# Kernel optimization log

Hardware: AMD Instinct MI355X
Metric: run time of the kernel (lower is better)

The kernel has to match this reference:

```python
import jax, jax.numpy as jnp
import numpy as np

HID = 2560
NH, P, N, G, K = 80, 64, 128, 1, 4
INTER = NH * P            # 5120
CONV_DIM = INTER + 2 * G * N  # 5376
PROJ = INTER + CONV_DIM + NH  # 10576
EPS = 1e-5
DT_MIN, DT_MAX = 0.0, 100.0
BATCH = 64


def setup_inputs() -> dict:
    key = jax.random.key(0)
    ks = jax.random.split(key, 11)
    return {
        "input_states": jax.random.normal(ks[0], (BATCH, 1, HID), jnp.float32),
        "conv_state": 0.1 * jax.random.normal(ks[1], (BATCH, CONV_DIM, K), jnp.float32),
        "ssm_state": 0.1 * jax.random.normal(ks[2], (BATCH, NH, P, N), jnp.float32),
        "in_proj_w": jax.random.normal(ks[3], (PROJ, HID), jnp.float32) * (HID ** -0.5),
        "conv_w": jax.random.normal(ks[4], (CONV_DIM, K), jnp.float32) * 0.2,
        "conv_b": jax.random.normal(ks[5], (CONV_DIM,), jnp.float32) * 0.02,
        "dt_bias": jax.random.normal(ks[6], (NH,), jnp.float32) * 0.1,
        "A_log": jnp.log(jnp.arange(1, NH + 1, dtype=jnp.float32)),
        "D": jnp.ones((NH,), jnp.float32),
        "norm_w": jnp.ones((INTER,), jnp.float32),
        "out_proj_w": jax.random.normal(ks[7], (HID, INTER), jnp.float32) * (INTER ** -0.5),
    }


def reference(input_states, conv_state, ssm_state, in_proj_w, conv_w, conv_b,
              dt_bias, A_log, D, norm_w, out_proj_w):
    B = input_states.shape[0]
    # in_proj: (B,1,HID) @ (HID,PROJ) -> (B,1,PROJ); d_mlp == 0 with these dims
    proj = jnp.einsum("bsh,ph->bsp", input_states, in_proj_w)
    gate = proj[..., :INTER]                       # (B,1,INTER)
    hBC = proj[..., INTER:INTER + CONV_DIM]        # (B,1,CONV_DIM)
    dt = proj[..., INTER + CONV_DIM:]              # (B,1,NH)

    # conv cache update: roll left, append current token
    new_conv_state = jnp.concatenate(
        [conv_state[:, :, 1:], hBC[:, 0, :, None]], axis=-1)  # (B,CONV_DIM,K)
    x = jnp.sum(new_conv_state * conv_w[None], axis=-1) + conv_b  # (B,CONV_DIM)
    x = jax.nn.silu(x)

    hs = x[:, :INTER].reshape(B, NH, P)            # (B,NH,P)
    Bm = x[:, INTER:INTER + G * N].reshape(B, G, N)
    Cm = x[:, INTER + G * N:].reshape(B, G, N)
    Bm = jnp.repeat(Bm, NH // G, axis=1)           # (B,NH,N)
    Cm = jnp.repeat(Cm, NH // G, axis=1)           # (B,NH,N)

    # discretization (dt is per-head, broadcast over head_dim as in source)
    dt_sp = jnp.clip(jax.nn.softplus(dt[:, 0, :] + dt_bias), DT_MIN, DT_MAX)  # (B,NH)
    A = -jnp.exp(A_log)                            # (NH,)
    dA = jnp.exp(dt_sp * A)                        # (B,NH)

    dBx = dt_sp[:, :, None, None] * Bm[:, :, None, :] * hs[..., None]  # (B,NH,P,N)
    new_ssm = ssm_state * dA[:, :, None, None] + dBx                   # (B,NH,P,N)

    y = jnp.einsum("bhpn,bhn->bhp", new_ssm, Cm)   # (B,NH,P)
    y = y + hs * D[None, :, None]
    y = y.reshape(B, 1, INTER)

    # gated RMSNorm (fp32 internals)
    yf = y.astype(jnp.float32) * jax.nn.silu(gate.astype(jnp.float32))
    var = jnp.mean(yf * yf, axis=-1, keepdims=True)
    yn = norm_w * (yf * jax.lax.rsqrt(var + EPS)).astype(y.dtype)

    out = jnp.einsum("bsi,hi->bsh", yn, out_proj_w)  # (B,1,HID)
    return out
```

## Files before the change

### kernel.cpp

```cpp
#include <hip/hip_runtime.h>
#include <stdint.h>

#define HID 2560
#define NH 80
#define PDIM 64
#define NDIM 128
#define INTER 5120
#define CONV_DIM 5376
#define PROJ_DIM 10576
#define NBATCH 64
#define EPS_ 1e-5f

typedef short short8 __attribute__((ext_vector_type(8)));
typedef float f32x4 __attribute__((ext_vector_type(4)));

__device__ __forceinline__ unsigned short f2bf(float f){
  unsigned u = __builtin_bit_cast(unsigned, f);
  u += 0x7FFFu + ((u >> 16) & 1u);
  return (unsigned short)(u >> 16);
}
__device__ __forceinline__ float silu_(float x){ return x / (1.f + __expf(-x)); }

__global__ __launch_bounds__(256) void k_dt(const float* __restrict__ X,
                                            const float* __restrict__ W,
                                            float* __restrict__ dt_part,
                                            unsigned short* __restrict__ Xb){
  const int h = blockIdx.x, ks = blockIdx.y;
  const int tid = threadIdx.x, wid = tid >> 6, lane = tid & 63;
  const float* wr = W + (size_t)(INTER + CONV_DIM + h) * HID + ks * 320;
  float w[5];
  #pragma unroll
  for (int i = 0; i < 5; ++i) w[i] = wr[lane + i * 64];
  #pragma unroll
  for (int bi = 0; bi < 16; ++bi){
    const int b = wid * 16 + bi;
    const float* xr = X + (size_t)b * HID + ks * 320;
    float x[5];
    float acc = 0.f;
    #pragma unroll
    for (int i = 0; i < 5; ++i){ x[i] = xr[lane + i * 64]; acc += x[i] * w[i]; }
    if (h == 0){
      #pragma unroll
      for (int i = 0; i < 5; ++i)
        Xb[(size_t)b * HID + ks * 320 + lane + i * 64] = f2bf(x[i]);
    }
    #pragma unroll
    for (int m = 32; m; m >>= 1) acc += __shfl_xor(acc, m);
    if (lane == 0) dt_part[(ks * NBATCH + b) * NH + h] = acc;
  }
}

__global__ __launch_bounds__(64, 1) void k1_proj(const unsigned short* __restrict__ Xb,
                                                 const float* __restrict__ W,
                                                 float* __restrict__ pp){
  const int lane = threadIdx.x;
  const int lr = lane & 15, lg = lane >> 4;
  const int n0 = blockIdx.x * 64;
  const int ks = blockIdx.y;
  const int kb = ks * 320;
  const short* ap = (const short*)Xb + (size_t)lr * HID + kb + lg * 8;
  const float* bp0; const float* bp1; const float* bp2; const float* bp3;
  {
    int r0 = n0;          if (r0 > PROJ_DIM - 16) r0 = PROJ_DIM - 16;
    int r1 = n0 + 16;     if (r1 > PROJ_DIM - 16) r1 = PROJ_DIM - 16;
    int r2 = n0 + 32;     if (r2 > PROJ_DIM - 16) r2 = PROJ_DIM - 16;
    int r3 = n0 + 48;     if (r3 > PROJ_DIM - 16) r3 = PROJ_DIM - 16;
    bp0 = W + (size_t)(r0 + lr) * HID + kb + lg * 8;
    bp1 = W + (size_t)(r1 + lr) * HID + kb + lg * 8;
    bp2 = W + (size_t)(r2 + lr) * HID + kb + lg * 8;
    bp3 = W + (size_t)(r3 + lr) * HID + kb + lg * 8;
  }
  f32x4 acc0[4], acc1[4], acc2[4], acc3[4];
  #pragma unroll
  for (int mt = 0; mt < 4; ++mt){
    acc0[mt] = (f32x4){0,0,0,0}; acc1[mt] = (f32x4){0,0,0,0};
    acc2[mt] = (f32x4){0,0,0,0}; acc3[mt] = (f32x4){0,0,0,0};
  }
  short8 A0[2], A1[2], A2[2], A3[2];
  float4 Bv0[2][2], Bv1[2][2], Bv2[2][2], Bv3[2][2];
  A0[0] = *(const short8*)(ap);
  A1[0] = *(const short8*)(ap + 16 * HID);
  A2[0] = *(const short8*)(ap + 32 * HID);
  A3[0] = *(const short8*)(ap + 48 * HID);
  Bv0[0][0] = *(const float4*)(bp0); Bv0[0][1] = *(const float4*)(bp0 + 4);
  Bv1[0][0] = *(const float4*)(bp1); Bv1[0][1] = *(const float4*)(bp1 + 4);
  Bv2[0][0] = *(const float4*)(bp2); Bv2[0][1] = *(const float4*)(bp2 + 4);
  Bv3[0][0] = *(const float4*)(bp3); Bv3[0][1] = *(const float4*)(bp3 + 4);
  #pragma unroll
  for (int s = 0; s < 10; ++s){
    const int p = s & 1;
    if (s + 1 < 10){
      const int k = (s + 1) * 32, q = p ^ 1;
      A0[q] = *(const short8*)(ap + k);
      A1[q] = *(const short8*)(ap + 16 * HID + k);
      A2[q] = *(const short8*)(ap + 32 * HID + k);
      A3[q] = *(const short8*)(ap + 48 * HID + k);
      Bv0[q][0] = *(const float4*)(bp0 + k); Bv0[q][1] = *(const float4*)(bp0 + k + 4);
      Bv1[q][0] = *(const float4*)(bp1 + k); Bv1[q][1] = *(const float4*)(bp1 + k + 4);
      Bv2[q][0] = *(const float4*)(bp2 + k); Bv2[q][1] = *(const float4*)(bp2 + k + 4);
      Bv3[q][0] = *(const float4*)(bp3 + k); Bv3[q][1] = *(const float4*)(bp3 + k + 4);
    }
    short8 bb0, bb1, bb2, bb3;
    bb0[0]=(short)f2bf(Bv0[p][0].x); bb0[1]=(short)f2bf(Bv0[p][0].y);
    bb0[2]=(short)f2bf(Bv0[p][0].z); bb0[3]=(short)f2bf(Bv0[p][0].w);
    bb0[4]=(short)f2bf(Bv0[p][1].x); bb0[5]=(short)f2bf(Bv0[p][1].y);
    bb0[6]=(short)f2bf(Bv0[p][1].z); bb0[7]=(short)f2bf(Bv0[p][1].w);
    bb1[0]=(short)f2bf(Bv1[p][0].x); bb1[1]=(short)f2bf(Bv1[p][0].y);
    bb1[2]=(short)f2bf(Bv1[p][0].z); bb1[3]=(short)f2bf(Bv1[p][0].w);
    bb1[4]=(short)f2bf(Bv1[p][1].x); bb1[5]=(short)f2bf(Bv1[p][1].y);
    bb1[6]=(short)f2bf(Bv1[p][1].z); bb1[7]=(short)f2bf(Bv1[p][1].w);
    bb2[0]=(short)f2bf(Bv2[p][0].x); bb2[1]=(short)f2bf(Bv2[p][0].y);
    bb2[2]=(short)f2bf(Bv2[p][0].z); bb2[3]=(short)f2bf(Bv2[p][0].w);
    bb2[4]=(short)f2bf(Bv2[p][1].x); bb2[5]=(short)f2bf(Bv2[p][1].y);
    bb2[6]=(short)f2bf(Bv2[p][1].z); bb2[7]=(short)f2bf(Bv2[p][1].w);
    bb3[0]=(short)f2bf(Bv3[p][0].x); bb3[1]=(short)f2bf(Bv3[p][0].y);
    bb3[2]=(short)f2bf(Bv3[p][0].z); bb3[3]=(short)f2bf(Bv3[p][0].w);
    bb3[4]=(short)f2bf(Bv3[p][1].x); bb3[5]=(short)f2bf(Bv3[p][1].y);
    bb3[6]=(short)f2bf(Bv3[p][1].z); bb3[7]=(short)f2bf(Bv3[p][1].w);
    acc0[0] = __builtin_amdgcn_mfma_f32_16x16x32_bf16(A0[p], bb0, acc0[0], 0, 0, 0);
    acc0[1] = __builtin_amdgcn_mfma_f32_16x16x32_bf16(A1[p], bb0, acc0[1], 0, 0, 0);
    acc0[2] = __builtin_amdgcn_mfma_f32_16x16x32_bf16(A2[p], bb0, acc0[2], 0, 0, 0);
    acc0[3] = __builtin_amdgcn_mfma_f32_16x16x32_bf16(A3[p], bb0, acc0[3], 0, 0, 0);
    acc1[0] = __builtin_amdgcn_mfma_f32_16x16x32_bf16(A0[p], bb1, acc1[0], 0, 0, 0);
    acc1[1] = __builtin_amdgcn_mfma_f32_16x16x32_bf16(A1[p], bb1, acc1[1], 0, 0, 0);
    acc1[2] = __builtin_amdgcn_mfma_f32_16x16x32_bf16(A2[p], bb1, acc1[2], 0, 0, 0);
    acc1[3] = __builtin_amdgcn_mfma_f32_16x16x32_bf16(A3[p], bb1, acc1[3], 0, 0, 0);
    acc2[0] = __builtin_amdgcn_mfma_f32_16x16x32_bf16(A0[p], bb2, acc2[0], 0, 0, 0);
    acc2[1] = __builtin_amdgcn_mfma_f32_16x16x32_bf16(A1[p], bb2, acc2[1], 0, 0, 0);
    acc2[2] = __builtin_amdgcn_mfma_f32_16x16x32_bf16(A2[p], bb2, acc2[2], 0, 0, 0);
    acc2[3] = __builtin_amdgcn_mfma_f32_16x16x32_bf16(A3[p], bb2, acc2[3], 0, 0, 0);
    acc3[0] = __builtin_amdgcn_mfma_f32_16x16x32_bf16(A0[p], bb3, acc3[0], 0, 0, 0);
    acc3[1] = __builtin_amdgcn_mfma_f32_16x16x32_bf16(A1[p], bb3, acc3[1], 0, 0, 0);
    acc3[2] = __builtin_amdgcn_mfma_f32_16x16x32_bf16(A2[p], bb3, acc3[2], 0, 0, 0);
    acc3[3] = __builtin_amdgcn_mfma_f32_16x16x32_bf16(A3[p], bb3, acc3[3], 0, 0, 0);
  }
  float* plane = pp + (size_t)ks * NBATCH * PROJ_DIM;
  #pragma unroll
  for (int mt = 0; mt < 4; ++mt){
    #pragma unroll
    for (int r = 0; r < 4; ++r){
      const int m = mt * 16 + lg * 4 + r;
      float* pm = plane + (size_t)m * PROJ_DIM;
      if (n0      < PROJ_DIM) pm[n0      + lr] = acc0[mt][r];
      if (n0 + 16 < PROJ_DIM) pm[n0 + 16 + lr] = acc1[mt][r];
      if (n0 + 32 < PROJ_DIM) pm[n0 + 32 + lr] = acc2[mt][r];
      if (n0 + 48 < PROJ_DIM) pm[n0 + 48 + lr] = acc3[mt][r];
    }
  }
}

__global__ __launch_bounds__(256) void k2a(const float* __restrict__ cs,
                                           const float* __restrict__ cw,
                                           const float* __restrict__ cb,
                                           const float* __restrict__ pp,
                                           const float* __restrict__ dt_part,
                                           const float* __restrict__ dt_bias,
                                           const float* __restrict__ A_log,
                                           float* __restrict__ hs_bc,
                                           float* __restrict__ dt_sp,
                                           float* __restrict__ dAv,
                                           float* __restrict__ s_bc){
  const int b = blockIdx.y;
  const int c0 = blockIdx.x * 384;
  const int tid = threadIdx.x;
  const size_t plane = (size_t)NBATCH * PROJ_DIM;
  __shared__ float bc[384];
  for (int i = tid; i < 384; i += 256){
    const int c = c0 + i;
    float4 s4 = *(const float4*)(cs + ((size_t)b * CONV_DIM + c) * 4);
    float4 w4 = *(const float4*)(cw + (size_t)c * 4);
    const size_t pidx = (size_t)b * PROJ_DIM + INTER + c;
    float hbc = 0.f;
    #pragma unroll
    for (int ks = 0; ks < 8; ++ks) hbc += pp[(size_t)ks * plane + pidx];
    float x = s4.y * w4.x + s4.z * w4.y + s4.w * w4.z + hbc * w4.w + cb[c];
    float v = silu_(x);
    hs_bc[(size_t)b * CONV_DIM + c] = v;
    if (blockIdx.x == 13) bc[i] = v;
  }
  if (blockIdx.x == 0 && tid < NH){
    float acc = dt_bias[tid];
    #pragma unroll
    for (int ks = 0; ks < 8; ++ks) acc += dt_part[(ks * NBATCH + b) * NH + tid];
    float sp = acc > 15.f ? acc : log1pf(__expf(acc));
    sp = fminf(fmaxf(sp, 0.f), 100.f);
    dt_sp[b * NH + tid] = sp;
    dAv[b * NH + tid] = __expf(-sp * __expf(A_log[tid]));
  }
  if (blockIdx.x == 13){
    __syncthreads();
    if (tid < 64){
      float p = bc[128 + tid] * bc[256 + tid] + bc[192 + tid] * bc[320 + tid];
      #pragma unroll
      for (int m = 32; m; m >>= 1) p += __shfl_xor(p, m);
      if (tid == 0) s_bc[b] = p;
    }
  }
}

__global__ __launch_bounds__(256) void k2b(const float* __restrict__ ssm,
                                           const float* __restrict__ hs_bc,
                                           const float* __restrict__ pp,
                                           const float* __restrict__ dt_sp,
                                           const float* __restrict__ dAv,
                                           const float* __restrict__ s_bc,
                                           const float* __restrict__ Dp,
                                           const float* __restrict__ norm_w,
                                           unsigned short* __restrict__ yfb,
                                           float* __restrict__ ssq_part){
  const int h = blockIdx.x, b = blockIdx.y;
  const int tid = threadIdx.x;
  const int wid = tid >> 6, lane = tid & 63;
  const int lr = lane & 15, lg = lane >> 4;
  const float dA_s = dAv[b * NH + h];
  const float coef = dt_sp[b * NH + h] * s_bc[b] + Dp[h];
  const size_t plane = (size_t)NBATCH * PROJ_DIM;
  const float* Cb = hs_bc + (size_t)b * CONV_DIM + INTER + NDIM;
  float4 c0 = *(const float4*)(Cb + lr * 8);
  float4 c1 = *(const float4*)(Cb + lr * 8 + 4);
  const float* srow = ssm + ((size_t)b * NH + h) * PDIM * NDIM;
  float ssq = 0.f;
  __shared__ float ssql[4];
  #pragma unroll
  for (int r = 0; r < 4; ++r){
    const int p = wid * 16 + r * 4 + lg;
    const float* sp_ = srow + (size_t)p * NDIM + lr * 8;
    float4 v0 = *(const float4*)(sp_);
    float4 v1 = *(const float4*)(sp_ + 4);
    float dot = v0.x*c0.x + v0.y*c0.y + v0.z*c0.z + v0.w*c0.w
              + v1.x*c1.x + v1.y*c1.y + v1.z*c1.z + v1.w*c1.w;
    dot += __shfl_xor(dot, 1); dot += __shfl_xor(dot, 2);
    dot += __shfl_xor(dot, 4); dot += __shfl_xor(dot, 8);
    if (lr == 0){
      const int hp = h * PDIM + p;
      float hs = hs_bc[(size_t)b * CONV_DIM + hp];
      float y = dA_s * dot + hs * coef;
      const size_t gi = (size_t)b * PROJ_DIM + hp;
      float g = 0.f;
      #pragma unroll
      for (int ks = 0; ks < 8; ++ks) g += pp[(size_t)ks * plane + gi];
      float yf = y * silu_(g) * norm_w[hp];
      yfb[(size_t)b * INTER + hp] = f2bf(yf);
      ssq += yf * yf;
    }
  }
  #pragma unroll
  for (int m = 32; m; m >>= 1) ssq += __shfl_xor(ssq, m);
  if (lane == 0) ssql[wid] = ssq;
  __syncthreads();
  if (tid == 0) ssq_part[b * NH + h] = ssql[0] + ssql[1] + ssql[2] + ssql[3];
}

__global__ __launch_bounds__(64, 1) void k3_out(const unsigned short* __restrict__ Yb,
                                                const float* __restrict__ W,
                                                float* __restrict__ part){
  const int lane = threadIdx.x;
  const int lr = lane & 15, lg = lane >> 4;
  const int n0 = blockIdx.x * 32;
  const int ks = blockIdx.y;
  const int kb = ks * 320;
  const short* ap = (const short*)Yb + (size_t)lr * INTER + kb + lg * 8;
  const float* bp0 = W + (size_t)(n0      + lr) * INTER + kb + lg * 8;
  const float* bp1 = W + (size_t)(n0 + 16 + lr) * INTER + kb + lg * 8;
  f32x4 acc0[4], acc1[4];
  #pragma unroll
  for (int mt = 0; mt < 4; ++mt){
    acc0[mt] = (f32x4){0,0,0,0}; acc1[mt] = (f32x4){0,0,0,0};
  }
  short8 A0[2], A1[2], A2[2], A3[2];
  float4 Bv0[2][2], Bv1[2][2];
  A0[0] = *(const short8*)(ap);
  A1[0] = *(const short8*)(ap + 16 * INTER);
  A2[0] = *(const short8*)(ap + 32 * INTER);
  A3[0] = *(const short8*)(ap + 48 * INTER);
  Bv0[0][0] = *(const float4*)(bp0); Bv0[0][1] = *(const float4*)(bp0 + 4);
  Bv1[0][0] = *(const float4*)(bp1); Bv1[0][1] = *(const float4*)(bp1 + 4);
  #pragma unroll
  for (int s = 0; s < 10; ++s){
    const int p = s & 1;
    if (s + 1 < 10){
      const int k = (s + 1) * 32, q = p ^ 1;
      A0[q] = *(const short8*)(ap + k);
      A1[q] = *(const short8*)(ap + 16 * INTER + k);
      A2[q] = *(const short8*)(ap + 32 * INTER + k);
      A3[q] = *(const short8*)(ap + 48 * INTER + k);
      Bv0[q][0] = *(const float4*)(bp0 + k); Bv0[q][1] = *(const float4*)(bp0 + k + 4);
      Bv1[q][0] = *(const float4*)(bp1 + k); Bv1[q][1] = *(const float4*)(bp1 + k + 4);
    }
    short8 bb0, bb1;
    bb0[0]=(short)f2bf(Bv0[p][0].x); bb0[1]=(short)f2bf(Bv0[p][0].y);
    bb0[2]=(short)f2bf(Bv0[p][0].z); bb0[3]=(short)f2bf(Bv0[p][0].w);
    bb0[4]=(short)f2bf(Bv0[p][1].x); bb0[5]=(short)f2bf(Bv0[p][1].y);
    bb0[6]=(short)f2bf(Bv0[p][1].z); bb0[7]=(short)f2bf(Bv0[p][1].w);
    bb1[0]=(short)f2bf(Bv1[p][0].x); bb1[1]=(short)f2bf(Bv1[p][0].y);
    bb1[2]=(short)f2bf(Bv1[p][0].z); bb1[3]=(short)f2bf(Bv1[p][0].w);
    bb1[4]=(short)f2bf(Bv1[p][1].x); bb1[5]=(short)f2bf(Bv1[p][1].y);
    bb1[6]=(short)f2bf(Bv1[p][1].z); bb1[7]=(short)f2bf(Bv1[p][1].w);
    acc0[0] = __builtin_amdgcn_mfma_f32_16x16x32_bf16(A0[p], bb0, acc0[0], 0, 0, 0);
    acc0[1] = __builtin_amdgcn_mfma_f32_16x16x32_bf16(A1[p], bb0, acc0[1], 0, 0, 0);
    acc0[2] = __builtin_amdgcn_mfma_f32_16x16x32_bf16(A2[p], bb0, acc0[2], 0, 0, 0);
    acc0[3] = __builtin_amdgcn_mfma_f32_16x16x32_bf16(A3[p], bb0, acc0[3], 0, 0, 0);
    acc1[0] = __builtin_amdgcn_mfma_f32_16x16x32_bf16(A0[p], bb1, acc1[0], 0, 0, 0);
    acc1[1] = __builtin_amdgcn_mfma_f32_16x16x32_bf16(A1[p], bb1, acc1[1], 0, 0, 0);
    acc1[2] = __builtin_amdgcn_mfma_f32_16x16x32_bf16(A2[p], bb1, acc1[2], 0, 0, 0);
    acc1[3] = __builtin_amdgcn_mfma_f32_16x16x32_bf16(A3[p], bb1, acc1[3], 0, 0, 0);
  }
  float* pt = part + (size_t)ks * NBATCH * 2560;
  #pragma unroll
  for (int mt = 0; mt < 4; ++mt){
    #pragma unroll
    for (int r = 0; r < 4; ++r){
      const int m = mt * 16 + lg * 4 + r;
      float* pm = pt + (size_t)m * 2560;
      pm[n0      + lr] = acc0[mt][r];
      pm[n0 + 16 + lr] = acc1[mt][r];
    }
  }
}

__global__ __launch_bounds__(256) void k4_norm(const float* __restrict__ part,
                                               const float* __restrict__ ssq_part,
                                               float* __restrict__ out){
  const int b = blockIdx.y;
  const int tid = threadIdx.x;
  __shared__ float w4[4];
  __shared__ float sc;
  float v = (tid < NH) ? ssq_part[b * NH + tid] : 0.f;
  #pragma unroll
  for (int m = 32; m; m >>= 1) v += __shfl_xor(v, m);
  const int wid = tid >> 6, lane = tid & 63;
  if (lane == 0) w4[wid] = v;
  __syncthreads();
  if (tid == 0){
    float total = w4[0] + w4[1] + w4[2] + w4[3];
    sc = rsqrtf(total / (float)INTER + EPS_);
  }
  __syncthreads();
  const int j = blockIdx.x * 256 + tid;
  const size_t idx = (size_t)b * 2560 + j;
  const size_t plane = (size_t)NBATCH * 2560;
  float s = 0.f;
  #pragma unroll
  for (int ks = 0; ks < 16; ++ks) s += part[(size_t)ks * plane + idx];
  out[idx] = sc * s;
}

extern "C" void kernel_launch(void* const* d_in, const int* in_sizes, int n_in,
                              void* d_out, int out_size, void* d_ws, size_t ws_size,
                              hipStream_t stream){
  const float* x_in       = (const float*)d_in[0];
  const float* conv_state = (const float*)d_in[1];
  const float* ssm_state  = (const float*)d_in[2];
  const float* in_proj_w  = (const float*)d_in[3];
  const float* conv_w     = (const float*)d_in[4];
  const float* conv_b     = (const float*)d_in[5];
  const float* dt_bias    = (const float*)d_in[6];
  const float* A_log      = (const float*)d_in[7];
  const float* Dp         = (const float*)d_in[8];
  const float* norm_w     = (const float*)d_in[9];
  const float* out_proj_w = (const float*)d_in[10];
  float* out = (float*)d_out;

  char* ws = (char*)d_ws;
  unsigned short* Xb   = (unsigned short*)(ws);
  float* dt_part       = (float*)(ws + 327680);
  float* pp            = (float*)(ws + 491520);
  float* hs_bc         = (float*)(ws + 22151168);
  float* dt_sp         = (float*)(ws + 23527424);
  float* dAv           = (float*)(ws + 23547904);
  float* s_bc          = (float*)(ws + 23568384);
  float* ssq           = (float*)(ws + 23568640);
  unsigned short* Yb   = (unsigned short*)(ws + 23589120);
  float* part          = (float*)(ws + 24244480);

  k_dt<<<dim3(NH, 8), dim3(256), 0, stream>>>(x_in, in_proj_w, dt_part, Xb);
  k1_proj<<<dim3(166, 8), dim3(64), 0, stream>>>(Xb, in_proj_w, pp);
  k2a<<<dim3(14, NBATCH), dim3(256), 0, stream>>>(conv_state, conv_w, conv_b, pp,
                                                  dt_part, dt_bias, A_log,
                                                  hs_bc, dt_sp, dAv, s_bc);
  k2b<<<dim3(NH, NBATCH), dim3(256), 0, stream>>>(ssm_state, hs_bc, pp, dt_sp, dAv,
                                                  s_bc, Dp, norm_w, Yb, ssq);
  k3_out<<<dim3(80, 16), dim3(64), 0, stream>>>(Yb, out_proj_w, part);
  k4_norm<<<dim3(10, NBATCH), dim3(256), 0, stream>>>(part, ssq, out);
}
```

Before: 123.7 us.

## Double split-K depth and store GEMM partial sums as bf16

Both projection GEMMs now use twice as many K-splits (16 and 32), so each block does half the K work and the grid has twice as many blocks to fill the GPU. The split-K partial planes are written as bf16 instead of fp32, which halves workspace traffic for the extra partials. The consumer kernels sum 16 or 32 bf16 partials. This trades accuracy, since each partial sum is rounded to bf16 before reduction, for more parallelism and less memory traffic.

```diff
diff --git a/kernel.cpp b/kernel.cpp
--- a/kernel.cpp
+++ b/kernel.cpp
@@ -19,6 +19,10 @@
   u += 0x7FFFu + ((u >> 16) & 1u);
   return (unsigned short)(u >> 16);
 }
+__device__ __forceinline__ float bf2f(unsigned short v){
+  unsigned x = (unsigned)v << 16;
+  return __builtin_bit_cast(float, x);
+}
 __device__ __forceinline__ float silu_(float x){ return x / (1.f + __expf(-x)); }
 
 __global__ __launch_bounds__(256) void k_dt(const float* __restrict__ X,
@@ -52,12 +56,12 @@
 
 __global__ __launch_bounds__(64, 1) void k1_proj(const unsigned short* __restrict__ Xb,
                                                  const float* __restrict__ W,
-                                                 float* __restrict__ pp){
+                                                 unsigned short* __restrict__ pp){
   const int lane = threadIdx.x;
   const int lr = lane & 15, lg = lane >> 4;
   const int n0 = blockIdx.x * 64;
   const int ks = blockIdx.y;
-  const int kb = ks * 320;
+  const int kb = ks * 160;
   const short* ap = (const short*)Xb + (size_t)lr * HID + kb + lg * 8;
   const float* bp0; const float* bp1; const float* bp2; const float* bp3;
   {
@@ -87,9 +91,9 @@
   Bv2[0][0] = *(const float4*)(bp2); Bv2[0][1] = *(const float4*)(bp2 + 4);
   Bv3[0][0] = *(const float4*)(bp3); Bv3[0][1] = *(const float4*)(bp3 + 4);
   #pragma unroll
-  for (int s = 0; s < 10; ++s){
+  for (int s = 0; s < 5; ++s){
     const int p = s & 1;
-    if (s + 1 < 10){
+    if (s + 1 < 5){
       const int k = (s + 1) * 32, q = p ^ 1;
       A0[q] = *(const short8*)(ap + k);
       A1[q] = *(const short8*)(ap + 16 * HID + k);
@@ -134,17 +138,17 @@
     acc3[2] = __builtin_amdgcn_mfma_f32_16x16x32_bf16(A2[p], bb3, acc3[2], 0, 0, 0);
     acc3[3] = __builtin_amdgcn_mfma_f32_16x16x32_bf16(A3[p], bb3, acc3[3], 0, 0, 0);
   }
-  float* plane = pp + (size_t)ks * NBATCH * PROJ_DIM;
+  unsigned short* plane = pp + (size_t)ks * NBATCH * PROJ_DIM;
   #pragma unroll
   for (int mt = 0; mt < 4; ++mt){
     #pragma unroll
     for (int r = 0; r < 4; ++r){
       const int m = mt * 16 + lg * 4 + r;
-      float* pm = plane + (size_t)m * PROJ_DIM;
-      if (n0      < PROJ_DIM) pm[n0      + lr] = acc0[mt][r];
-      if (n0 + 16 < PROJ_DIM) pm[n0 + 16 + lr] = acc1[mt][r];
-      if (n0 + 32 < PROJ_DIM) pm[n0 + 32 + lr] = acc2[mt][r];
-      if (n0 + 48 < PROJ_DIM) pm[n0 + 48 + lr] = acc3[mt][r];
+      unsigned short* pm = plane + (size_t)m * PROJ_DIM;
+      if (n0      < PROJ_DIM) pm[n0      + lr] = f2bf(acc0[mt][r]);
+      if (n0 + 16 < PROJ_DIM) pm[n0 + 16 + lr] = f2bf(acc1[mt][r]);
+      if (n0 + 32 < PROJ_DIM) pm[n0 + 32 + lr] = f2bf(acc2[mt][r]);
+      if (n0 + 48 < PROJ_DIM) pm[n0 + 48 + lr] = f2bf(acc3[mt][r]);
     }
   }
 }
@@ -152,7 +156,7 @@
 __global__ __launch_bounds__(256) void k2a(const float* __restrict__ cs,
                                            const float* __restrict__ cw,
                                            const float* __restrict__ cb,
-                                           const float* __restrict__ pp,
+                                           const unsigned short* __restrict__ pp,
                                            const float* __restrict__ dt_part,
                                            const float* __restrict__ dt_bias,
                                            const float* __restrict__ A_log,
@@ -172,7 +176,7 @@
     const size_t pidx = (size_t)b * PROJ_DIM + INTER + c;
     float hbc = 0.f;
     #pragma unroll
-    for (int ks = 0; ks < 8; ++ks) hbc += pp[(size_t)ks * plane + pidx];
+    for (int ks = 0; ks < 16; ++ks) hbc += bf2f(pp[(size_t)ks * plane + pidx]);
     float x = s4.y * w4.x + s4.z * w4.y + s4.w * w4.z + hbc * w4.w + cb[c];
     float v = silu_(x);
     hs_bc[(size_t)b * CONV_DIM + c] = v;
@@ -200,7 +204,7 @@
 
 __global__ __launch_bounds__(256) void k2b(const float* __restrict__ ssm,
                                            const float* __restrict__ hs_bc,
-                                           const float* __restrict__ pp,
+                                           const unsigned short* __restrict__ pp,
                                            const float* __restrict__ dt_sp,
                                            const float* __restrict__ dAv,
                                            const float* __restrict__ s_bc,
@@ -238,7 +242,7 @@
       const size_t gi = (size_t)b * PROJ_DIM + hp;
       float g = 0.f;
       #pragma unroll
-      for (int ks = 0; ks < 8; ++ks) g += pp[(size_t)ks * plane + gi];
+      for (int ks = 0; ks < 16; ++ks) g += bf2f(pp[(size_t)ks * plane + gi]);
       float yf = y * silu_(g) * norm_w[hp];
       yfb[(size_t)b * INTER + hp] = f2bf(yf);
       ssq += yf * yf;
@@ -253,12 +257,12 @@
 
 __global__ __launch_bounds__(64, 1) void k3_out(const unsigned short* __restrict__ Yb,
                                                 const float* __restrict__ W,
-                                                float* __restrict__ part){
+                                                unsigned short* __restrict__ part){
   const int lane = threadIdx.x;
   const int lr = lane & 15, lg = lane >> 4;
   const int n0 = blockIdx.x * 32;
   const int ks = blockIdx.y;
-  const int kb = ks * 320;
+  const int kb = ks * 160;
   const short* ap = (const short*)Yb + (size_t)lr * INTER + kb + lg * 8;
   const float* bp0 = W + (size_t)(n0      + lr) * INTER + kb + lg * 8;
   const float* bp1 = W + (size_t)(n0 + 16 + lr) * INTER + kb + lg * 8;
@@ -276,9 +280,9 @@
   Bv0[0][0] = *(const float4*)(bp0); Bv0[0][1] = *(const float4*)(bp0 + 4);
   Bv1[0][0] = *(const float4*)(bp1); Bv1[0][1] = *(const float4*)(bp1 + 4);
   #pragma unroll
-  for (int s = 0; s < 10; ++s){
+  for (int s = 0; s < 5; ++s){
     const int p = s & 1;
-    if (s + 1 < 10){
+    if (s + 1 < 5){
       const int k = (s + 1) * 32, q = p ^ 1;
       A0[q] = *(const short8*)(ap + k);
       A1[q] = *(const short8*)(ap + 16 * INTER + k);
@@ -305,20 +309,20 @@
     acc1[2] = __builtin_amdgcn_mfma_f32_16x16x32_bf16(A2[p], bb1, acc1[2], 0, 0, 0);
     acc1[3] = __builtin_amdgcn_mfma_f32_16x16x32_bf16(A3[p], bb1, acc1[3], 0, 0, 0);
   }
-  float* pt = part + (size_t)ks * NBATCH * 2560;
+  unsigned short* pt = part + (size_t)ks * NBATCH * 2560;
   #pragma unroll
   for (int mt = 0; mt < 4; ++mt){
     #pragma unroll
     for (int r = 0; r < 4; ++r){
       const int m = mt * 16 + lg * 4 + r;
-      float* pm = pt + (size_t)m * 2560;
-      pm[n0      + lr] = acc0[mt][r];
-      pm[n0 + 16 + lr] = acc1[mt][r];
-    }
-  }
-}
-
-__global__ __launch_bounds__(256) void k4_norm(const float* __restrict__ part,
+      unsigned short* pm = pt + (size_t)m * 2560;
+      pm[n0      + lr] = f2bf(acc0[mt][r]);
+      pm[n0 + 16 + lr] = f2bf(acc1[mt][r]);
+    }
+  }
+}
+
+__global__ __launch_bounds__(256) void k4_norm(const unsigned short* __restrict__ part,
                                                const float* __restrict__ ssq_part,
                                                float* __restrict__ out){
   const int b = blockIdx.y;
@@ -341,7 +345,7 @@
   const size_t plane = (size_t)NBATCH * 2560;
   float s = 0.f;
   #pragma unroll
-  for (int ks = 0; ks < 16; ++ks) s += part[(size_t)ks * plane + idx];
+  for (int ks = 0; ks < 32; ++ks) s += bf2f(part[(size_t)ks * plane + idx]);
   out[idx] = sc * s;
 }
 
@@ -364,22 +368,22 @@
   char* ws = (char*)d_ws;
   unsigned short* Xb   = (unsigned short*)(ws);
   float* dt_part       = (float*)(ws + 327680);
-  float* pp            = (float*)(ws + 491520);
+  unsigned short* pp   = (unsigned short*)(ws + 491520);
   float* hs_bc         = (float*)(ws + 22151168);
   float* dt_sp         = (float*)(ws + 23527424);
   float* dAv           = (float*)(ws + 23547904);
   float* s_bc          = (float*)(ws + 23568384);
   float* ssq           = (float*)(ws + 23568640);
   unsigned short* Yb   = (unsigned short*)(ws + 23589120);
-  float* part          = (float*)(ws + 24244480);
+  unsigned short* part = (unsigned short*)(ws + 24244480);
 
   k_dt<<<dim3(NH, 8), dim3(256), 0, stream>>>(x_in, in_proj_w, dt_part, Xb);
-  k1_proj<<<dim3(166, 8), dim3(64), 0, stream>>>(Xb, in_proj_w, pp);
+  k1_proj<<<dim3(166, 16), dim3(64), 0, stream>>>(Xb, in_proj_w, pp);
   k2a<<<dim3(14, NBATCH), dim3(256), 0, stream>>>(conv_state, conv_w, conv_b, pp,
                                                   dt_part, dt_bias, A_log,
                                                   hs_bc, dt_sp, dAv, s_bc);
   k2b<<<dim3(NH, NBATCH), dim3(256), 0, stream>>>(ssm_state, hs_bc, pp, dt_sp, dAv,
                                                   s_bc, Dp, norm_w, Yb, ssq);
-  k3_out<<<dim3(80, 16), dim3(64), 0, stream>>>(Yb, out_proj_w, part);
+  k3_out<<<dim3(80, 32), dim3(64), 0, stream>>>(Yb, out_proj_w, part);
   k4_norm<<<dim3(10, NBATCH), dim3(256), 0, stream>>>(part, ssq, out);
 }
```

Result: slower. 129.5 us (+4.7%).
